# Kernel optimization log

Hardware: AMD Instinct MI355X
Metric: run time of the kernel (lower is better)

The kernel has to match this reference:

```python
import jax, jax.numpy as jnp
import numpy as np

B, L, D, V, U = 4096, 50, 64, 100000, 256
E = 2 * D          # concat of two seq-feature embeddings
CAT = 3 * E        # concat([q, k, q*k])


def setup_inputs() -> dict:
    key = jax.random.key(0)
    ks = jax.random.split(key, 12)
    inp = {
        "query_ids_item": jax.random.randint(ks[0], (B, 1), 0, V),
        "query_ids_cate": jax.random.randint(ks[1], (B, 1), 0, V),
        "seq_ids_item": jax.random.randint(ks[2], (B, 1, L), 0, V),
        "seq_ids_cate": jax.random.randint(ks[3], (B, 1, L), 0, V),
        "mask": jax.random.randint(ks[4], (B, 1, L), 0, 2).astype(bool),
        # learned params
        "emb_item": jax.random.normal(ks[5], (V, D), jnp.float32) * 0.05,
        "emb_cate": jax.random.normal(ks[6], (V, D), jnp.float32) * 0.05,
        "W_hide": jax.random.normal(ks[7], (CAT, U), jnp.float32) * (1.0 / np.sqrt(CAT)),
        "b_hide": jnp.zeros((U,), jnp.float32),
        "W_out": jax.random.normal(ks[8], (U, 1), jnp.float32) * (1.0 / np.sqrt(U)),
        "b_out": jnp.zeros((1,), jnp.float32),
    }
    return inp


def reference(query_ids_item, query_ids_cate, seq_ids_item, seq_ids_cate, mask,
              emb_item, emb_cate, W_hide, b_hide, W_out, b_out):
    # Embedding gathers (StdOneHot per seq feature, concat over features)
    q = jnp.concatenate([emb_item[query_ids_item], emb_cate[query_ids_cate]], axis=-1)   # [B,1,E]
    k = jnp.concatenate([emb_item[seq_ids_item], emb_cate[seq_ids_cate]], axis=-1)        # [B,1,L,E]

    # DinAttention: tile query over L, concat([q, k, q*k])
    qt = jnp.broadcast_to(q[:, :, None, :], k.shape)                                       # [B,1,L,E]
    cat = jnp.concatenate([qt, k, qt * k], axis=-1)                                        # [B,1,L,3E]

    h = jax.nn.relu(jnp.einsum('bglc,cu->bglu', cat, W_hide) + b_hide)                     # [B,1,L,U]
    scores = jnp.einsum('bglu,uo->bglo', h, W_out) + b_out                                 # [B,1,L,1]
    scores = jnp.swapaxes(scores, -1, -2)                                                  # [B,1,1,L]

    # mask [B,1,L] -> expand_dims axis=1 -> [B,1,1,L]; multiply (no softmax)
    scores = scores * mask.astype(jnp.float32)[:, None, :, :].reshape(mask.shape[0], 1, 1, -1)

    out = jnp.einsum('bgol,bgle->bgoe', scores, k)                                         # [B,1,1,E]
    return jnp.squeeze(out, axis=-2)                                                       # [B,1,E]
```

## Files before the change

### kernel.cpp

```cpp
#include <hip/hip_runtime.h>
#include <hip/hip_bf16.h>


#define L_SEQ 50
#define LP    64
#define D_EMB 64
#define E_DIM 128
#define U_DIM 256
#define CATK  384
#define V_SZ  100000
#define KSTR  136

typedef __bf16 bf16x2 __attribute__((ext_vector_type(2)));
typedef __bf16 bf16x4 __attribute__((ext_vector_type(4)));
typedef __bf16 bf16x8 __attribute__((ext_vector_type(8)));
typedef float  f32x4  __attribute__((ext_vector_type(4)));

__device__ __bf16 g_W3[65536];
__device__ __bf16 g_Wq_c[128 * 256];

__global__ __launch_bounds__(256) void prep_kernel(const float* __restrict__ W_hide) {
  const int bid = blockIdx.x, t = threadIdx.x;
  if (bid < 32) {
    const int base = bid * 1024;
#pragma unroll
    for (int i = 0; i < 4; ++i) {
      int idx = base + i * 256 + t;
      g_Wq_c[idx] = (__bf16)W_hide[idx];
    }
  } else {
    const int o = (bid - 32) * 256 + t;
    const int s = o >> 10, ut = (o >> 6) & 15, lane = o & 63;
    const int quad = lane >> 4, m = lane & 15;
    const int u = ut * 16 + m;
    const int c0 = 128 + s * 32 + quad * 8;
    bf16x8 v;
#pragma unroll
    for (int j = 0; j < 8; ++j)
      v[j] = (__bf16)W_hide[(c0 + j) * 256 + u];
    *(bf16x8*)&g_W3[o * 8] = v;
  }
}

__global__ __launch_bounds__(256) void din_main_kernel(
    const int* __restrict__ qid_item, const int* __restrict__ qid_cate,
    const int* __restrict__ seq_item, const int* __restrict__ seq_cate,
    const int* __restrict__ mask,
    const float* __restrict__ emb_item,
    const float* __restrict__ emb_cate,
    const float* __restrict__ b_hide,
    const float* __restrict__ W_out,
    const float* __restrict__ b_out,
    float* __restrict__ out) {
  __shared__ alignas(16) __bf16 Kb[LP * KSTR];
  __shared__ alignas(16) __bf16 A2[LP * KSTR];
  __shared__ alignas(16) float qrowf[E_DIM];
  __shared__ alignas(16) float qv2[2][U_DIM];
  __shared__ float mask_f[LP];
  __shared__ float scpart[4][LP];
  __shared__ float scores_s[LP];
  __shared__ float outp[4][E_DIM];

  const int b = blockIdx.x;
  const int t = threadIdx.x;
  const int r = t >> 2, q4 = t & 3;
  const int col0 = q4 * 32;

  float4 kv[8];
  if (r < L_SEQ) {
    int id = (q4 < 2) ? seq_item[b * L_SEQ + r] : seq_cate[b * L_SEQ + r];
    if ((unsigned)id >= (unsigned)V_SZ) id = 0;
    const float4* s4 = (const float4*)(((q4 < 2) ? emb_item : emb_cate)
                                       + (size_t)id * D_EMB + (q4 & 1) * 32);
#pragma unroll
    for (int i = 0; i < 8; ++i) kv[i] = s4[i];
  } else {
#pragma unroll
    for (int i = 0; i < 8; ++i) kv[i] = make_float4(0.f, 0.f, 0.f, 0.f);
  }
#pragma unroll
  for (int i = 0; i < 8; ++i) {
    bf16x4 h4 = {(__bf16)kv[i].x, (__bf16)kv[i].y, (__bf16)kv[i].z, (__bf16)kv[i].w};
    *(bf16x4*)&Kb[r * KSTR + col0 + i * 4] = h4;
  }
  if (t < 4) {
    int id = (t < 2) ? qid_item[b] : qid_cate[b];
    if ((unsigned)id >= (unsigned)V_SZ) id = 0;
    const float4* s4 = (const float4*)(((t < 2) ? emb_item : emb_cate)
                                       + (size_t)id * D_EMB + (t & 1) * 32);
    float4* d4 = (float4*)&qrowf[t * 32];
#pragma unroll
    for (int i = 0; i < 8; ++i) d4[i] = s4[i];
  }
  if (t < LP) mask_f[t] = (t < L_SEQ && mask[b * L_SEQ + t] != 0) ? 1.0f : 0.0f;
  __syncthreads();

#pragma unroll
  for (int i = 0; i < 8; ++i) {
    const float* qp = &qrowf[col0 + i * 4];
    bf16x4 h4 = {(__bf16)(kv[i].x * qp[0]), (__bf16)(kv[i].y * qp[1]),
                 (__bf16)(kv[i].z * qp[2]), (__bf16)(kv[i].w * qp[3])};
    *(bf16x4*)&A2[r * KSTR + col0 + i * 4] = h4;
  }
  __syncthreads();

  {
    const int ch = t >> 7;
    const int u0 = (t & 127) * 2;
    float a0 = ch ? 0.f : b_hide[u0];
    float a1 = ch ? 0.f : b_hide[u0 + 1];
    const __bf16* wp = &g_Wq_c[(ch * 64) * 256 + u0];
    const float* qp = &qrowf[ch * 64];
#pragma unroll 16
    for (int cc = 0; cc < 64; ++cc) {
      bf16x2 w2 = *(const bf16x2*)(wp + cc * 256);
      float qc = qp[cc];
      a0 += qc * (float)w2[0];
      a1 += qc * (float)w2[1];
    }
    qv2[ch][u0] = a0;
    qv2[ch][u0 + 1] = a1;
  }

  const int wave = t >> 6, lane = t & 63;
  const int m = lane & 15, quad = lane >> 4;
  f32x4 acc[4][4];
#pragma unroll
  for (int mt = 0; mt < 4; ++mt)
#pragma unroll
    for (int nt = 0; nt < 4; ++nt) acc[mt][nt] = (f32x4){0.f, 0.f, 0.f, 0.f};

#pragma unroll
  for (int s = 0; s < 8; ++s) {
    const __bf16* Bb = (s < 4) ? Kb : A2;
    const int klocal = (s & 3) * 32 + quad * 8;
    bf16x8 wfr[4], kfr[4];
#pragma unroll
    for (int mt = 0; mt < 4; ++mt) {
      const int o = s * 1024 + (wave * 4 + mt) * 64 + lane;
      wfr[mt] = *(const bf16x8*)&g_W3[o * 8];
    }
#pragma unroll
    for (int nt = 0; nt < 4; ++nt)
      kfr[nt] = *(const bf16x8*)&Bb[(nt * 16 + m) * KSTR + klocal];
#pragma unroll
    for (int mt = 0; mt < 4; ++mt)
#pragma unroll
      for (int nt = 0; nt < 4; ++nt)
        acc[mt][nt] = __builtin_amdgcn_mfma_f32_16x16x32_bf16(
            wfr[mt], kfr[nt], acc[mt][nt], 0, 0, 0);
  }
  __syncthreads();

  float qv4[4][4], wo4[4][4];
#pragma unroll
  for (int mt = 0; mt < 4; ++mt) {
    const int u0 = wave * 64 + mt * 16 + quad * 4;
    f32x4 qa = *(const f32x4*)&qv2[0][u0];
    f32x4 qb = *(const f32x4*)&qv2[1][u0];
    float4 ww = *(const float4*)&W_out[u0];
    qv4[mt][0] = qa[0] + qb[0]; qv4[mt][1] = qa[1] + qb[1];
    qv4[mt][2] = qa[2] + qb[2]; qv4[mt][3] = qa[3] + qb[3];
    wo4[mt][0] = ww.x;  wo4[mt][1] = ww.y;  wo4[mt][2] = ww.z;  wo4[mt][3] = ww.w;
  }
  float part[4];
#pragma unroll
  for (int nt = 0; nt < 4; ++nt) {
    float sum = 0.f;
#pragma unroll
    for (int mt = 0; mt < 4; ++mt)
#pragma unroll
      for (int rg = 0; rg < 4; ++rg) {
        float h = acc[mt][nt][rg] + qv4[mt][rg];
        h = fmaxf(h, 0.f);
        sum += h * wo4[mt][rg];
      }
    part[nt] = sum;
  }
#pragma unroll
  for (int nt = 0; nt < 4; ++nt) {
    part[nt] += __shfl_xor(part[nt], 16, 64);
    part[nt] += __shfl_xor(part[nt], 32, 64);
  }
  if (lane < 16) {
#pragma unroll
    for (int nt = 0; nt < 4; ++nt)
      scpart[wave][nt * 16 + lane] = part[nt];
  }
  __syncthreads();

  if (t < LP) {
    float s = scpart[0][t] + scpart[1][t] + scpart[2][t] + scpart[3][t]
            + b_out[0];
    scores_s[t] = s * mask_f[t];
  }
  __syncthreads();
  {
    const int e2 = lane * 2;
    float o0 = 0.f, o1 = 0.f;
#pragma unroll
    for (int i = 0; i < 16; ++i) {
      const int l = wave * 16 + i;
      const float sc = scores_s[l];
      bf16x2 kk = *(const bf16x2*)&Kb[l * KSTR + e2];
      o0 += sc * (float)kk[0];
      o1 += sc * (float)kk[1];
    }
    outp[wave][e2]     = o0;
    outp[wave][e2 + 1] = o1;
  }
  __syncthreads();
  if (t < E_DIM) {
    float o = outp[0][t] + outp[1][t] + outp[2][t] + outp[3][t];
    out[(size_t)b * E_DIM + t] = o;
  }
}

extern "C" void kernel_launch(void* const* d_in, const int* in_sizes, int n_in,
                              void* d_out, int out_size, void* d_ws, size_t ws_size,
                              hipStream_t stream) {
  const int* qid_item = (const int*)d_in[0];
  const int* qid_cate = (const int*)d_in[1];
  const int* seq_item = (const int*)d_in[2];
  const int* seq_cate = (const int*)d_in[3];
  const int* mask     = (const int*)d_in[4];
  const float* emb_item = (const float*)d_in[5];
  const float* emb_cate = (const float*)d_in[6];
  const float* W_hide   = (const float*)d_in[7];
  const float* b_hide   = (const float*)d_in[8];
  const float* W_out    = (const float*)d_in[9];
  const float* b_out    = (const float*)d_in[10];
  float* out = (float*)d_out;

  (void)d_ws; (void)ws_size;

  prep_kernel<<<64, 256, 0, stream>>>(W_hide);
  din_main_kernel<<<4096, 256, 0, stream>>>(qid_item, qid_cate, seq_item, seq_cate,
                                            mask, emb_item, emb_cate,
                                            b_hide, W_out, b_out, out);
}
```

Baseline: 161.7 us.

## Process multiple batches per block with software-prefetched embedding gathers

Each block now handles NB=4 batch rows in a loop, and the grid shrinks to 1024 blocks. The indices and embedding rows for the next batch are loaded into registers while the current batch's MFMA and reduction run, so gather latency can overlap compute. The cost is higher register pressure, since an extra float4[8] buffer stays live across the MFMA loop, which can lower occupancy. There are also fewer blocks to spread across the CUs.

```diff
diff --git a/kernel.cpp b/kernel.cpp
--- a/kernel.cpp
+++ b/kernel.cpp
@@ -10,6 +10,7 @@
 #define CATK  384
 #define V_SZ  100000
 #define KSTR  136
+#define NB    4
 
 typedef __bf16 bf16x2 __attribute__((ext_vector_type(2)));
 typedef __bf16 bf16x4 __attribute__((ext_vector_type(4)));
@@ -61,158 +62,221 @@
   __shared__ float scores_s[LP];
   __shared__ float outp[4][E_DIM];
 
-  const int b = blockIdx.x;
+  const int b0 = blockIdx.x * NB;
   const int t = threadIdx.x;
   const int r = t >> 2, q4 = t & 3;
   const int col0 = q4 * 32;
-
-  float4 kv[8];
+  const int wave = t >> 6, lane = t & 63;
+  const int m = lane & 15, quad = lane >> 4;
+  const int rr = (r < L_SEQ) ? r : 0;
+
+  int sid, qidv = 0, mkv;
+  float4 kvp[8];
+  float4 qrp = make_float4(0.f, 0.f, 0.f, 0.f);
+
+  sid = (q4 < 2 ? seq_item : seq_cate)[b0 * L_SEQ + rr];
+  if (t < 32) qidv = (t < 16 ? qid_item : qid_cate)[b0];
+  mkv = (t < L_SEQ) ? mask[b0 * L_SEQ + t] : 0;
+
   if (r < L_SEQ) {
-    int id = (q4 < 2) ? seq_item[b * L_SEQ + r] : seq_cate[b * L_SEQ + r];
-    if ((unsigned)id >= (unsigned)V_SZ) id = 0;
+    int id = sid; if ((unsigned)id >= (unsigned)V_SZ) id = 0;
     const float4* s4 = (const float4*)(((q4 < 2) ? emb_item : emb_cate)
                                        + (size_t)id * D_EMB + (q4 & 1) * 32);
 #pragma unroll
-    for (int i = 0; i < 8; ++i) kv[i] = s4[i];
+    for (int i2 = 0; i2 < 8; ++i2) kvp[i2] = s4[i2];
   } else {
 #pragma unroll
-    for (int i = 0; i < 8; ++i) kv[i] = make_float4(0.f, 0.f, 0.f, 0.f);
-  }
-#pragma unroll
-  for (int i = 0; i < 8; ++i) {
-    bf16x4 h4 = {(__bf16)kv[i].x, (__bf16)kv[i].y, (__bf16)kv[i].z, (__bf16)kv[i].w};
-    *(bf16x4*)&Kb[r * KSTR + col0 + i * 4] = h4;
-  }
-  if (t < 4) {
-    int id = (t < 2) ? qid_item[b] : qid_cate[b];
-    if ((unsigned)id >= (unsigned)V_SZ) id = 0;
-    const float4* s4 = (const float4*)(((t < 2) ? emb_item : emb_cate)
-                                       + (size_t)id * D_EMB + (t & 1) * 32);
-    float4* d4 = (float4*)&qrowf[t * 32];
-#pragma unroll
-    for (int i = 0; i < 8; ++i) d4[i] = s4[i];
-  }
-  if (t < LP) mask_f[t] = (t < L_SEQ && mask[b * L_SEQ + t] != 0) ? 1.0f : 0.0f;
+    for (int i2 = 0; i2 < 8; ++i2) kvp[i2] = make_float4(0.f, 0.f, 0.f, 0.f);
+  }
+  if (t < 32) {
+    int id = qidv; if ((unsigned)id >= (unsigned)V_SZ) id = 0;
+    qrp = *(const float4*)(((t < 16) ? emb_item : emb_cate)
+                           + (size_t)id * D_EMB + (t & 15) * 4);
+  }
+  int mk_cur = mkv;
+  if (NB > 1) {
+    sid = (q4 < 2 ? seq_item : seq_cate)[(b0 + 1) * L_SEQ + rr];
+    if (t < 32) qidv = (t < 16 ? qid_item : qid_cate)[b0 + 1];
+    mkv = (t < L_SEQ) ? mask[(b0 + 1) * L_SEQ + t] : 0;
+  }
+#pragma unroll
+  for (int i2 = 0; i2 < 8; ++i2) {
+    bf16x4 h4 = {(__bf16)kvp[i2].x, (__bf16)kvp[i2].y,
+                 (__bf16)kvp[i2].z, (__bf16)kvp[i2].w};
+    *(bf16x4*)&Kb[r * KSTR + col0 + i2 * 4] = h4;
+  }
+  if (t < 32) *(float4*)&qrowf[(t < 16 ? 0 : 64) + (t & 15) * 4] = qrp;
+  if (t < LP) mask_f[t] = (t < L_SEQ && mk_cur != 0) ? 1.0f : 0.0f;
   __syncthreads();
-
-#pragma unroll
-  for (int i = 0; i < 8; ++i) {
-    const float* qp = &qrowf[col0 + i * 4];
-    bf16x4 h4 = {(__bf16)(kv[i].x * qp[0]), (__bf16)(kv[i].y * qp[1]),
-                 (__bf16)(kv[i].z * qp[2]), (__bf16)(kv[i].w * qp[3])};
-    *(bf16x4*)&A2[r * KSTR + col0 + i * 4] = h4;
+#pragma unroll
+  for (int i2 = 0; i2 < 8; ++i2) {
+    const float* qp = &qrowf[col0 + i2 * 4];
+    bf16x4 h4 = {(__bf16)(kvp[i2].x * qp[0]), (__bf16)(kvp[i2].y * qp[1]),
+                 (__bf16)(kvp[i2].z * qp[2]), (__bf16)(kvp[i2].w * qp[3])};
+    *(bf16x4*)&A2[r * KSTR + col0 + i2 * 4] = h4;
   }
   __syncthreads();
 
-  {
-    const int ch = t >> 7;
-    const int u0 = (t & 127) * 2;
-    float a0 = ch ? 0.f : b_hide[u0];
-    float a1 = ch ? 0.f : b_hide[u0 + 1];
-    const __bf16* wp = &g_Wq_c[(ch * 64) * 256 + u0];
-    const float* qp = &qrowf[ch * 64];
+  for (int i = 0; i < NB; ++i) {
+    const int b = b0 + i;
+    const bool more = (i + 1 < NB);
+    float4 kq[8];
+    float4 qq = make_float4(0.f, 0.f, 0.f, 0.f);
+    int mq = 0;
+
+    if (more) {
+      if (r < L_SEQ) {
+        int id = sid; if ((unsigned)id >= (unsigned)V_SZ) id = 0;
+        const float4* s4 = (const float4*)(((q4 < 2) ? emb_item : emb_cate)
+                                           + (size_t)id * D_EMB + (q4 & 1) * 32);
+#pragma unroll
+        for (int i2 = 0; i2 < 8; ++i2) kq[i2] = s4[i2];
+      } else {
+#pragma unroll
+        for (int i2 = 0; i2 < 8; ++i2) kq[i2] = make_float4(0.f, 0.f, 0.f, 0.f);
+      }
+      if (t < 32) {
+        int id = qidv; if ((unsigned)id >= (unsigned)V_SZ) id = 0;
+        qq = *(const float4*)(((t < 16) ? emb_item : emb_cate)
+                              + (size_t)id * D_EMB + (t & 15) * 4);
+      }
+      mq = mkv;
+      if (i + 2 < NB) {
+        sid = (q4 < 2 ? seq_item : seq_cate)[(b + 2) * L_SEQ + rr];
+        if (t < 32) qidv = (t < 16 ? qid_item : qid_cate)[b + 2];
+        mkv = (t < L_SEQ) ? mask[(b + 2) * L_SEQ + t] : 0;
+      }
+    }
+
+    {
+      const int ch = t >> 7;
+      const int u0 = (t & 127) * 2;
+      float a0 = ch ? 0.f : b_hide[u0];
+      float a1 = ch ? 0.f : b_hide[u0 + 1];
+      const __bf16* wp = &g_Wq_c[(ch * 64) * 256 + u0];
+      const float* qp = &qrowf[ch * 64];
 #pragma unroll 16
-    for (int cc = 0; cc < 64; ++cc) {
-      bf16x2 w2 = *(const bf16x2*)(wp + cc * 256);
-      float qc = qp[cc];
-      a0 += qc * (float)w2[0];
-      a1 += qc * (float)w2[1];
-    }
-    qv2[ch][u0] = a0;
-    qv2[ch][u0 + 1] = a1;
-  }
-
-  const int wave = t >> 6, lane = t & 63;
-  const int m = lane & 15, quad = lane >> 4;
-  f32x4 acc[4][4];
-#pragma unroll
-  for (int mt = 0; mt < 4; ++mt)
-#pragma unroll
-    for (int nt = 0; nt < 4; ++nt) acc[mt][nt] = (f32x4){0.f, 0.f, 0.f, 0.f};
-
-#pragma unroll
-  for (int s = 0; s < 8; ++s) {
-    const __bf16* Bb = (s < 4) ? Kb : A2;
-    const int klocal = (s & 3) * 32 + quad * 8;
-    bf16x8 wfr[4], kfr[4];
+      for (int cc = 0; cc < 64; ++cc) {
+        bf16x2 w2 = *(const bf16x2*)(wp + cc * 256);
+        float qc = qp[cc];
+        a0 += qc * (float)w2[0];
+        a1 += qc * (float)w2[1];
+      }
+      qv2[ch][u0] = a0;
+      qv2[ch][u0 + 1] = a1;
+    }
+
+    f32x4 acc[4][4];
+#pragma unroll
+    for (int mt = 0; mt < 4; ++mt)
+#pragma unroll
+      for (int nt = 0; nt < 4; ++nt) acc[mt][nt] = (f32x4){0.f, 0.f, 0.f, 0.f};
+
+#pragma unroll
+    for (int s = 0; s < 8; ++s) {
+      const __bf16* Bb = (s < 4) ? Kb : A2;
+      const int klocal = (s & 3) * 32 + quad * 8;
+      bf16x8 wfr[4], kfr[4];
+#pragma unroll
+      for (int mt = 0; mt < 4; ++mt) {
+        const int o = s * 1024 + (wave * 4 + mt) * 64 + lane;
+        wfr[mt] = *(const bf16x8*)&g_W3[o * 8];
+      }
+#pragma unroll
+      for (int nt = 0; nt < 4; ++nt)
+        kfr[nt] = *(const bf16x8*)&Bb[(nt * 16 + m) * KSTR + klocal];
+#pragma unroll
+      for (int mt = 0; mt < 4; ++mt)
+#pragma unroll
+        for (int nt = 0; nt < 4; ++nt)
+          acc[mt][nt] = __builtin_amdgcn_mfma_f32_16x16x32_bf16(
+              wfr[mt], kfr[nt], acc[mt][nt], 0, 0, 0);
+    }
+    __syncthreads();
+
+    float qv4[4][4], wo4[4][4];
 #pragma unroll
     for (int mt = 0; mt < 4; ++mt) {
-      const int o = s * 1024 + (wave * 4 + mt) * 64 + lane;
-      wfr[mt] = *(const bf16x8*)&g_W3[o * 8];
-    }
-#pragma unroll
-    for (int nt = 0; nt < 4; ++nt)
-      kfr[nt] = *(const bf16x8*)&Bb[(nt * 16 + m) * KSTR + klocal];
-#pragma unroll
-    for (int mt = 0; mt < 4; ++mt)
+      const int u0 = wave * 64 + mt * 16 + quad * 4;
+      f32x4 qa = *(const f32x4*)&qv2[0][u0];
+      f32x4 qb = *(const f32x4*)&qv2[1][u0];
+      float4 ww = *(const float4*)&W_out[u0];
+      qv4[mt][0] = qa[0] + qb[0]; qv4[mt][1] = qa[1] + qb[1];
+      qv4[mt][2] = qa[2] + qb[2]; qv4[mt][3] = qa[3] + qb[3];
+      wo4[mt][0] = ww.x;  wo4[mt][1] = ww.y;  wo4[mt][2] = ww.z;  wo4[mt][3] = ww.w;
+    }
+    float part[4];
+#pragma unroll
+    for (int nt = 0; nt < 4; ++nt) {
+      float sum = 0.f;
+#pragma unroll
+      for (int mt = 0; mt < 4; ++mt)
+#pragma unroll
+        for (int rg = 0; rg < 4; ++rg) {
+          float h = acc[mt][nt][rg] + qv4[mt][rg];
+          h = fmaxf(h, 0.f);
+          sum += h * wo4[mt][rg];
+        }
+      part[nt] = sum;
+    }
+#pragma unroll
+    for (int nt = 0; nt < 4; ++nt) {
+      part[nt] += __shfl_xor(part[nt], 16, 64);
+      part[nt] += __shfl_xor(part[nt], 32, 64);
+    }
+    if (lane < 16) {
 #pragma unroll
       for (int nt = 0; nt < 4; ++nt)
-        acc[mt][nt] = __builtin_amdgcn_mfma_f32_16x16x32_bf16(
-            wfr[mt], kfr[nt], acc[mt][nt], 0, 0, 0);
-  }
-  __syncthreads();
-
-  float qv4[4][4], wo4[4][4];
-#pragma unroll
-  for (int mt = 0; mt < 4; ++mt) {
-    const int u0 = wave * 64 + mt * 16 + quad * 4;
-    f32x4 qa = *(const f32x4*)&qv2[0][u0];
-    f32x4 qb = *(const f32x4*)&qv2[1][u0];
-    float4 ww = *(const float4*)&W_out[u0];
-    qv4[mt][0] = qa[0] + qb[0]; qv4[mt][1] = qa[1] + qb[1];
-    qv4[mt][2] = qa[2] + qb[2]; qv4[mt][3] = qa[3] + qb[3];
-    wo4[mt][0] = ww.x;  wo4[mt][1] = ww.y;  wo4[mt][2] = ww.z;  wo4[mt][3] = ww.w;
-  }
-  float part[4];
-#pragma unroll
-  for (int nt = 0; nt < 4; ++nt) {
-    float sum = 0.f;
-#pragma unroll
-    for (int mt = 0; mt < 4; ++mt)
-#pragma unroll
-      for (int rg = 0; rg < 4; ++rg) {
-        float h = acc[mt][nt][rg] + qv4[mt][rg];
-        h = fmaxf(h, 0.f);
-        sum += h * wo4[mt][rg];
-      }
-    part[nt] = sum;
-  }
-#pragma unroll
-  for (int nt = 0; nt < 4; ++nt) {
-    part[nt] += __shfl_xor(part[nt], 16, 64);
-    part[nt] += __shfl_xor(part[nt], 32, 64);
-  }
-  if (lane < 16) {
-#pragma unroll
-    for (int nt = 0; nt < 4; ++nt)
-      scpart[wave][nt * 16 + lane] = part[nt];
-  }
-  __syncthreads();
-
-  if (t < LP) {
-    float s = scpart[0][t] + scpart[1][t] + scpart[2][t] + scpart[3][t]
-            + b_out[0];
-    scores_s[t] = s * mask_f[t];
-  }
-  __syncthreads();
-  {
-    const int e2 = lane * 2;
-    float o0 = 0.f, o1 = 0.f;
-#pragma unroll
-    for (int i = 0; i < 16; ++i) {
-      const int l = wave * 16 + i;
-      const float sc = scores_s[l];
-      bf16x2 kk = *(const bf16x2*)&Kb[l * KSTR + e2];
-      o0 += sc * (float)kk[0];
-      o1 += sc * (float)kk[1];
-    }
-    outp[wave][e2]     = o0;
-    outp[wave][e2 + 1] = o1;
-  }
-  __syncthreads();
-  if (t < E_DIM) {
-    float o = outp[0][t] + outp[1][t] + outp[2][t] + outp[3][t];
-    out[(size_t)b * E_DIM + t] = o;
+        scpart[wave][nt * 16 + lane] = part[nt];
+    }
+    __syncthreads();
+
+    if (t < LP) {
+      float s = scpart[0][t] + scpart[1][t] + scpart[2][t] + scpart[3][t]
+              + b_out[0];
+      scores_s[t] = s * mask_f[t];
+    }
+    __syncthreads();
+
+    {
+      const int e2 = lane * 2;
+      float o0 = 0.f, o1 = 0.f;
+#pragma unroll
+      for (int i2 = 0; i2 < 16; ++i2) {
+        const int l = wave * 16 + i2;
+        const float sc = scores_s[l];
+        bf16x2 kk = *(const bf16x2*)&Kb[l * KSTR + e2];
+        o0 += sc * (float)kk[0];
+        o1 += sc * (float)kk[1];
+      }
+      outp[wave][e2]     = o0;
+      outp[wave][e2 + 1] = o1;
+    }
+    __syncthreads();
+
+    if (t < E_DIM) {
+      float o = outp[0][t] + outp[1][t] + outp[2][t] + outp[3][t];
+      out[(size_t)b * E_DIM + t] = o;
+    }
+    if (more) {
+#pragma unroll
+      for (int i2 = 0; i2 < 8; ++i2) {
+        bf16x4 h4 = {(__bf16)kq[i2].x, (__bf16)kq[i2].y,
+                     (__bf16)kq[i2].z, (__bf16)kq[i2].w};
+        *(bf16x4*)&Kb[r * KSTR + col0 + i2 * 4] = h4;
+      }
+      if (t < 32) *(float4*)&qrowf[(t < 16 ? 0 : 64) + (t & 15) * 4] = qq;
+      if (t < LP) mask_f[t] = (t < L_SEQ && mq != 0) ? 1.0f : 0.0f;
+      __syncthreads();
+#pragma unroll
+      for (int i2 = 0; i2 < 8; ++i2) {
+        const float* qp = &qrowf[col0 + i2 * 4];
+        bf16x4 h4 = {(__bf16)(kq[i2].x * qp[0]), (__bf16)(kq[i2].y * qp[1]),
+                     (__bf16)(kq[i2].z * qp[2]), (__bf16)(kq[i2].w * qp[3])};
+        *(bf16x4*)&A2[r * KSTR + col0 + i2 * 4] = h4;
+      }
+      __syncthreads();
+    }
   }
 }
 
@@ -235,7 +299,7 @@
   (void)d_ws; (void)ws_size;
 
   prep_kernel<<<64, 256, 0, stream>>>(W_hide);
-  din_main_kernel<<<4096, 256, 0, stream>>>(qid_item, qid_cate, seq_item, seq_cate,
-                                            mask, emb_item, emb_cate,
-                                            b_hide, W_out, b_out, out);
+  din_main_kernel<<<4096 / NB, 256, 0, stream>>>(qid_item, qid_cate, seq_item,
+                                                 seq_cate, mask, emb_item, emb_cate,
+                                                 b_hide, W_out, b_out, out);
 }
```

Result: slower. 196.0 us (+21.3%).

## Precompute query projection in a batched kernel, remove it from main kernel

Applied to the files above, without the earlier changes.

Moves the per-batch query·W_q projection (plus bias) out of the main attention kernel into a separate kernel that processes 16 batch rows per block, reusing each W_hide load across 16 queries. The main kernel reads the precomputed vector from global memory, which lets it drop a shared buffer and a barrier. It also adds an occupancy hint of 4 blocks per SM. The cost is an extra launch and a 4MB intermediate buffer written and read through global memory.

```diff
diff --git a/kernel.cpp b/kernel.cpp
--- a/kernel.cpp
+++ b/kernel.cpp
@@ -9,6 +9,7 @@
 #define U_DIM 256
 #define CATK  384
 #define V_SZ  100000
+#define B_TOT 4096
 #define KSTR  136
 
 typedef __bf16 bf16x2 __attribute__((ext_vector_type(2)));
@@ -17,45 +18,81 @@
 typedef float  f32x4  __attribute__((ext_vector_type(4)));
 
 __device__ __bf16 g_W3[65536];
-__device__ __bf16 g_Wq_c[128 * 256];
+__device__ float  g_QV[B_TOT * U_DIM];
 
 __global__ __launch_bounds__(256) void prep_kernel(const float* __restrict__ W_hide) {
-  const int bid = blockIdx.x, t = threadIdx.x;
-  if (bid < 32) {
-    const int base = bid * 1024;
-#pragma unroll
-    for (int i = 0; i < 4; ++i) {
-      int idx = base + i * 256 + t;
-      g_Wq_c[idx] = (__bf16)W_hide[idx];
+  const int o = blockIdx.x * 256 + threadIdx.x;
+  const int s = o >> 10, ut = (o >> 6) & 15, lane = o & 63;
+  const int quad = lane >> 4, m = lane & 15;
+  const int u = ut * 16 + m;
+  const int c0 = 128 + s * 32 + quad * 8;
+  bf16x8 v;
+#pragma unroll
+  for (int j = 0; j < 8; ++j)
+    v[j] = (__bf16)W_hide[(c0 + j) * 256 + u];
+  *(bf16x8*)&g_W3[o * 8] = v;
+}
+
+__global__ __launch_bounds__(256) void qv_prep_kernel(
+    const int* __restrict__ qid_item, const int* __restrict__ qid_cate,
+    const float* __restrict__ emb_item, const float* __restrict__ emb_cate,
+    const float* __restrict__ W_hide, const float* __restrict__ b_hide) {
+  __shared__ float qs[16][E_DIM];
+  __shared__ float qvp[2][16][U_DIM];
+  const int b0 = blockIdx.x * 16;
+  const int t = threadIdx.x;
+#pragma unroll
+  for (int j = 0; j < 2; ++j) {
+    const int idx = j * 256 + t;
+    const int bs = idx >> 5, seg = idx & 31;
+    int id = (seg < 16 ? qid_item : qid_cate)[b0 + bs];
+    if ((unsigned)id >= (unsigned)V_SZ) id = 0;
+    const float4* s4 = (const float4*)(((seg < 16) ? emb_item : emb_cate)
+                                       + (size_t)id * D_EMB + (seg & 15) * 4);
+    *(float4*)&qs[bs][(seg < 16 ? 0 : 64) + (seg & 15) * 4] = *s4;
+  }
+  __syncthreads();
+  const int ch = t >> 7, u0 = (t & 127) * 2;
+  float a0[16], a1[16];
+#pragma unroll
+  for (int bs = 0; bs < 16; ++bs) {
+    a0[bs] = ch ? 0.f : b_hide[u0];
+    a1[bs] = ch ? 0.f : b_hide[u0 + 1];
+  }
+  const float* wrow = W_hide + (ch * 64) * 256 + u0;
+  for (int cc = 0; cc < 64; ++cc) {
+    const float w0 = (float)(__bf16)wrow[cc * 256];
+    const float w1 = (float)(__bf16)wrow[cc * 256 + 1];
+#pragma unroll
+    for (int bs = 0; bs < 16; ++bs) {
+      const float qc = qs[bs][ch * 64 + cc];
+      a0[bs] += qc * w0;
+      a1[bs] += qc * w1;
     }
-  } else {
-    const int o = (bid - 32) * 256 + t;
-    const int s = o >> 10, ut = (o >> 6) & 15, lane = o & 63;
-    const int quad = lane >> 4, m = lane & 15;
-    const int u = ut * 16 + m;
-    const int c0 = 128 + s * 32 + quad * 8;
-    bf16x8 v;
-#pragma unroll
-    for (int j = 0; j < 8; ++j)
-      v[j] = (__bf16)W_hide[(c0 + j) * 256 + u];
-    *(bf16x8*)&g_W3[o * 8] = v;
-  }
-}
-
-__global__ __launch_bounds__(256) void din_main_kernel(
+  }
+#pragma unroll
+  for (int bs = 0; bs < 16; ++bs) {
+    qvp[ch][bs][u0]     = a0[bs];
+    qvp[ch][bs][u0 + 1] = a1[bs];
+  }
+  __syncthreads();
+#pragma unroll
+  for (int bs = 0; bs < 16; ++bs)
+    g_QV[(size_t)(b0 + bs) * U_DIM + t] = qvp[0][bs][t] + qvp[1][bs][t];
+}
+
+__global__ __launch_bounds__(256, 4) void din_main_kernel(
     const int* __restrict__ qid_item, const int* __restrict__ qid_cate,
     const int* __restrict__ seq_item, const int* __restrict__ seq_cate,
     const int* __restrict__ mask,
     const float* __restrict__ emb_item,
     const float* __restrict__ emb_cate,
-    const float* __restrict__ b_hide,
     const float* __restrict__ W_out,
     const float* __restrict__ b_out,
     float* __restrict__ out) {
   __shared__ alignas(16) __bf16 Kb[LP * KSTR];
   __shared__ alignas(16) __bf16 A2[LP * KSTR];
   __shared__ alignas(16) float qrowf[E_DIM];
-  __shared__ alignas(16) float qv2[2][U_DIM];
   __shared__ float mask_f[LP];
   __shared__ float scpart[4][LP];
   __shared__ float scores_s[LP];
@@ -104,24 +141,6 @@
   }
   __syncthreads();
 
-  {
-    const int ch = t >> 7;
-    const int u0 = (t & 127) * 2;
-    float a0 = ch ? 0.f : b_hide[u0];
-    float a1 = ch ? 0.f : b_hide[u0 + 1];
-    const __bf16* wp = &g_Wq_c[(ch * 64) * 256 + u0];
-    const float* qp = &qrowf[ch * 64];
-#pragma unroll 16
-    for (int cc = 0; cc < 64; ++cc) {
-      bf16x2 w2 = *(const bf16x2*)(wp + cc * 256);
-      float qc = qp[cc];
-      a0 += qc * (float)w2[0];
-      a1 += qc * (float)w2[1];
-    }
-    qv2[ch][u0] = a0;
-    qv2[ch][u0 + 1] = a1;
-  }
-
   const int wave = t >> 6, lane = t & 63;
   const int m = lane & 15, quad = lane >> 4;
   f32x4 acc[4][4];
@@ -150,17 +169,14 @@
         acc[mt][nt] = __builtin_amdgcn_mfma_f32_16x16x32_bf16(
             wfr[mt], kfr[nt], acc[mt][nt], 0, 0, 0);
   }
-  __syncthreads();
 
   float qv4[4][4], wo4[4][4];
 #pragma unroll
   for (int mt = 0; mt < 4; ++mt) {
     const int u0 = wave * 64 + mt * 16 + quad * 4;
-    f32x4 qa = *(const f32x4*)&qv2[0][u0];
-    f32x4 qb = *(const f32x4*)&qv2[1][u0];
+    f32x4 qq = *(const f32x4*)&g_QV[(size_t)b * U_DIM + u0];
     float4 ww = *(const float4*)&W_out[u0];
-    qv4[mt][0] = qa[0] + qb[0]; qv4[mt][1] = qa[1] + qb[1];
-    qv4[mt][2] = qa[2] + qb[2]; qv4[mt][3] = qa[3] + qb[3];
+    qv4[mt][0] = qq[0]; qv4[mt][1] = qq[1]; qv4[mt][2] = qq[2]; qv4[mt][3] = qq[3];
     wo4[mt][0] = ww.x;  wo4[mt][1] = ww.y;  wo4[mt][2] = ww.z;  wo4[mt][3] = ww.w;
   }
   float part[4];
@@ -234,8 +250,11 @@
 
   (void)d_ws; (void)ws_size;
 
-  prep_kernel<<<64, 256, 0, stream>>>(W_hide);
-  din_main_kernel<<<4096, 256, 0, stream>>>(qid_item, qid_cate, seq_item, seq_cate,
-                                            mask, emb_item, emb_cate,
-                                            b_hide, W_out, b_out, out);
-}
+  prep_kernel<<<32, 256, 0, stream>>>(W_hide);
+  qv_prep_kernel<<<B_TOT / 16, 256, 0, stream>>>(qid_item, qid_cate,
+                                                 emb_item, emb_cate,
+                                                 W_hide, b_hide);
+  din_main_kernel<<<B_TOT, 256, 0, stream>>>(qid_item, qid_cate, seq_item,
+                                             seq_cate, mask, emb_item, emb_cate,
+                                             W_out, b_out, out);
+}
```

Result: slower. 170.0 us (+5.1%).
